# Optimization experiments

Measured on AMD Instinct MI355X. Metric: run time of the kernel, lower is better.

## Reference

```python
import jax, jax.numpy as jnp
import numpy as np

L, H, R, N, E = 6, 128, 64, 10000, 160000
SSILU_SCALE = 1.0 / 0.6  # ScaledSiLU
INV_SQRT_3 = 1.0 / np.sqrt(3.0)
INV_SQRT_H = 1.0 / np.sqrt(H)
INV_SQRT_2 = 1.0 / np.sqrt(2.0)


def ssilu(x):
    return jax.nn.silu(x) * SSILU_SCALE


def lnorm(x, w, b):
    m = x.mean(-1, keepdims=True)
    v = jnp.var(x, axis=-1, keepdims=True)
    return (x - m) * jax.lax.rsqrt(v + 1e-5) * w + b


def gated_block(x, v, wv1, wv2, wu1, bu1, wu2, bu2, hout):
    # GatedEquivariantBlock: x [N,Hin], v [N,3,Hin]
    vec1 = jnp.linalg.norm(jnp.einsum('nci,io->nco', v, wv1), axis=-2)  # [N,Hin]
    vec2 = jnp.einsum('nci,io->nco', v, wv2)                            # [N,3,hout]
    h = ssilu(jnp.concatenate([x, vec1], -1) @ wu1 + bu1) @ wu2 + bu2   # [N,2*hout]
    xs, xv = h[..., :hout], h[..., hout:]
    return ssilu(xs), xv[:, None, :] * vec2


def forward_impl(edge_index, x, vec, edge_rbf, edge_vector,
                 ln_w, ln_b, xp1_w, xp1_b, xp2_w, xp2_b, rbf_w, rbf_b,
                 vp_w, xv1_w, xv1_b, xv2_w, xv2_b,
                 we1, be1, we2, be2,
                 g1_v1, g1_v2, g1_u1, g1_u1b, g1_u2, g1_u2b,
                 g2_v1, g2_v2, g2_u1, g2_u1b, g2_u2, g2_u2b):
    src, dst = edge_index[0], edge_index[1]  # message flows src(j) -> dst(i)
    for l in range(L):
        # ---- PaiNNMessage ----
        xh = ssilu(lnorm(x, ln_w[l], ln_b[l]) @ xp1_w[l] + xp1_b[l]) @ xp2_w[l] + xp2_b[l]  # [N,3H]
        rbfh = edge_rbf @ rbf_w[l] + rbf_b[l]                                                # [E,3H]
        m = xh[src] * rbfh                                                                    # gather + elementwise
        mx = m[:, :H]
        m2 = m[:, H:2 * H] * INV_SQRT_3
        m3 = m[:, 2 * H:]
        mvec = (vec[src] * m2[:, None, :] + m3[:, None, :] * edge_vector[:, :, None]) * INV_SQRT_H  # [E,3,H]
        dx = jax.ops.segment_sum(mx, dst, num_segments=N)
        dvec = jax.ops.segment_sum(mvec, dst, num_segments=N)
        x = (x + dx) * INV_SQRT_2
        vec = vec + dvec
        # ---- PaiNNUpdate ----
        vp = jnp.einsum('nci,io->nco', vec, vp_w[l])  # [N,3,2H]
        v1, v2 = vp[..., :H], vp[..., H:]
        vec_dot = (v1 * v2).sum(axis=1) * INV_SQRT_H  # [N,H]
        vnorm = jnp.sqrt((v2 ** 2).sum(axis=-2) + 1e-8)
        h = ssilu(jnp.concatenate([x, vnorm], -1) @ xv1_w[l] + xv1_b[l]) @ xv2_w[l] + xv2_b[l]  # [N,3H]
        xu1, xu2, xu3 = h[:, :H], h[:, H:2 * H], h[:, 2 * H:]
        x = x + (xu1 + xu2 * vec_dot) * INV_SQRT_2
        vec = vec + xu3[:, None, :] * v1
        # ScaleFactor is identity without a scale file
    energy = ssilu(x @ we1 + be1) @ we2 + be2  # [N,1] per-atom energy
    fx, fv = gated_block(x, vec, g1_v1, g1_v2, g1_u1, g1_u1b, g1_u2, g1_u2b, H // 2)
    fx, fv = gated_block(fx, fv, g2_v1, g2_v2, g2_u1, g2_u1b, g2_u2, g2_u2b, 1)
    forces = fv[..., 0]  # [N,3]
    return jnp.concatenate([energy, forces], axis=-1)  # [N,4] packed (energy, fx, fy, fz)


def setup_inputs() -> dict:
    key = jax.random.key(0)
    ks = iter(jax.random.split(key, 64))
    nrm = lambda shape, s=0.05: jax.random.normal(next(ks), shape, jnp.float32) * s
    return dict(
        x=jax.random.normal(next(ks), (N, H), jnp.float32),
        vec=jax.random.normal(next(ks), (N, 3, H), jnp.float32),
        edge_index=jax.random.randint(next(ks), (2, E), 0, N),
        edge_rbf=jax.random.uniform(next(ks), (E, R), jnp.float32),
        edge_vector=jax.random.normal(next(ks), (E, 3), jnp.float32),
        ln_w=jnp.ones((L, H)), ln_b=jnp.zeros((L, H)),
        xp1_w=nrm((L, H, H)), xp1_b=jnp.zeros((L, H)),
        xp2_w=nrm((L, H, 3 * H)), xp2_b=jnp.zeros((L, 3 * H)),
        rbf_w=nrm((L, R, 3 * H)), rbf_b=jnp.zeros((L, 3 * H)),
        vp_w=nrm((L, H, 2 * H)),
        xv1_w=nrm((L, 2 * H, H)), xv1_b=jnp.zeros((L, H)),
        xv2_w=nrm((L, H, 3 * H)), xv2_b=jnp.zeros((L, 3 * H)),
        we1=nrm((H, H // 2)), be1=jnp.zeros((H // 2,)),
        we2=nrm((H // 2, 1)), be2=jnp.zeros((1,)),
        g1_v1=nrm((H, H)), g1_v2=nrm((H, H // 2)),
        g1_u1=nrm((2 * H, H)), g1_u1b=jnp.zeros((H,)),
        g1_u2=nrm((H, H)), g1_u2b=jnp.zeros((H,)),
        g2_v1=nrm((H // 2, H // 2)), g2_v2=nrm((H // 2, 1)),
        g2_u1=nrm((H, H // 2)), g2_u1b=jnp.zeros((H // 2,)),
        g2_u2=nrm((H // 2, 2)), g2_u2b=jnp.zeros((2,)),
    )


def reference(x, vec, edge_index, edge_rbf, edge_vector,
              ln_w, ln_b, xp1_w, xp1_b, xp2_w, xp2_b, rbf_w, rbf_b,
              vp_w, xv1_w, xv1_b, xv2_w, xv2_b,
              we1, be1, we2, be2,
              g1_v1, g1_v2, g1_u1, g1_u1b, g1_u2, g1_u2b,
              g2_v1, g2_v2, g2_u1, g2_u1b, g2_u2, g2_u2b):
    return forward_impl(edge_index, x, vec, edge_rbf, edge_vector,
                        ln_w, ln_b, xp1_w, xp1_b, xp2_w, xp2_b, rbf_w, rbf_b,
                        vp_w, xv1_w, xv1_b, xv2_w, xv2_b,
                        we1, be1, we2, be2,
                        g1_v1, g1_v2, g1_u1, g1_u1b, g1_u2, g1_u2b,
                        g2_v1, g2_v2, g2_u1, g2_u1b, g2_u2, g2_u2b)
```

## Files before the change

kernel.cpp:

```cpp
#include <hip/hip_runtime.h>
#include <hip/hip_bf16.h>

#define NN 10000
#define EE 160000
#define LL 6

#define INV_SQRT_3f  0.57735026919f
#define INV_SQRT_Hf  0.08838834764832f
#define INV_SQRT_2f  0.70710678118655f

typedef _Float16 half8 __attribute__((ext_vector_type(8)));
typedef float f32x4 __attribute__((ext_vector_type(4)));

#define WE1OFF   0
#define WV1OFF   8192
#define WV2OFF   24576
#define WU1OFF   32768
#define WU2OFF   65536
#define G2V1OFF  81920
#define G2U1OFF  86016
#define WFIN_SZ  94208

__device__ __forceinline__ float ssilu_f(float v){
  float s = 1.0f / (1.0f + __expf(-v));
  return v * s * 1.6666666666667f;
}
__device__ __forceinline__ float bcast(float v, int l){
  return __int_as_float(__builtin_amdgcn_readlane(__float_as_int(v), l));
}

__global__ __launch_bounds__(256) void k_hist(const int* __restrict__ edst, int* __restrict__ cnt){
  int i = blockIdx.x*256 + threadIdx.x;
  if (i < EE) atomicAdd(&cnt[edst[i]], 1);
}

__global__ __launch_bounds__(1024) void k_scan(const int* __restrict__ cnt,
                                               int* __restrict__ off, int* __restrict__ cur){
  __shared__ int ps[1024];
  int t = threadIdx.x;
  int base = t*10;
  int local[10];
  int s = 0;
  #pragma unroll
  for (int i=0;i<10;i++){
    int c = (base+i < NN) ? cnt[base+i] : 0;
    local[i] = s; s += c;
  }
  ps[t] = s;
  __syncthreads();
  for (int d=1; d<1024; d<<=1){
    int v = (t>=d) ? ps[t-d] : 0;
    __syncthreads();
    ps[t] += v;
    __syncthreads();
  }
  int pre = (t>0) ? ps[t-1] : 0;
  #pragma unroll
  for (int i=0;i<10;i++){
    int idx = base+i;
    if (idx < NN){ int o = pre + local[i]; off[idx]=o; cur[idx]=o; }
  }
  if (t==1023) off[NN] = ps[1023];
}

__global__ __launch_bounds__(256) void k_fill(const int* __restrict__ edst,
                                              int* __restrict__ cur, int* __restrict__ eord){
  int i = blockIdx.x*256 + threadIdx.x;
  if (i < EE){
    int d = edst[i];
    int p = atomicAdd(&cur[d], 1);
    eord[p] = i;
  }
}

__global__ __launch_bounds__(256) void k_sorta(const float* __restrict__ erbf,
                                               const int* __restrict__ eord, _Float16* __restrict__ eA){
  long i = (long)blockIdx.x*256 + threadIdx.x;
  if (i >= (long)EE*64) return;
  int j = i & 7, lane = (i >> 3) & 63, kh = (i >> 9) & 1;
  long tile = i >> 10;
  int e = eord[tile*16 + (lane&15)];
  eA[i] = (_Float16)erbf[(size_t)e*64 + kh*32 + (lane>>4)*8 + j];
}

__global__ __launch_bounds__(256) void k_sorte(const int* __restrict__ esrc, const float* __restrict__ evec,
                                               const int* __restrict__ eord, float4* __restrict__ es4){
  int p = blockIdx.x*256 + threadIdx.x;
  if (p >= EE) return;
  int e = eord[p];
  es4[p] = make_float4(evec[(size_t)e*3], evec[(size_t)e*3+1], evec[(size_t)e*3+2],
                       __int_as_float(esrc[e]));
}

__global__ __launch_bounds__(256) void k_packw(const float* __restrict__ w, _Float16* __restrict__ wf){
  int i = blockIdx.x*256 + threadIdx.x;
  if (i >= LL*24*2*64*8) return;
  int j    = i & 7;
  int lane = (i >> 3) & 63;
  int kh   = (i >> 9) & 1;
  int rest = i >> 10;
  int nb   = rest % 24;
  int l    = rest / 24;
  int k    = 32*kh + 8*(lane>>4) + j;
  int ch   = nb*16 + (lane&15);
  float v = w[((size_t)l*64 + k)*384 + ch];
  if (ch >= 128 && ch < 256) v *= INV_SQRT_3f;
  wf[i] = (_Float16)v;
}

__global__ __launch_bounds__(256) void k_packb(const float* __restrict__ b, float* __restrict__ bsc){
  int i = blockIdx.x*256 + threadIdx.x;
  if (i >= LL*384) return;
  int ch = i % 384;
  float v = b[i];
  if (ch >= 128 && ch < 256) v *= INV_SQRT_3f;
  bsc[i] = v;
}

struct PackTab {
  const float* s[40];
  _Float16* d[40];
  int K[40];
  int NO[40];
};
__global__ __launch_bounds__(256) void k_packall(PackTab tb){
  int e = blockIdx.y;
  int K = tb.K[e], NO = tb.NO[e];
  int tot = K*NO, KS = K >> 5;
  const float* s = tb.s[e];
  _Float16* d = tb.d[e];
  for (int i = blockIdx.x*256 + threadIdx.x; i < tot; i += gridDim.x*256){
    int j = i & 7, lane = (i >> 3) & 63, rest = i >> 9;
    int ks = rest % KS, nb = rest / KS;
    int k = ks*32 + (lane>>4)*8 + j, n = nb*16 + (lane&15);
    d[i] = (_Float16)s[(size_t)k*NO + n];
  }
}

__global__ __launch_bounds__(256) void k_cvt16(const float* __restrict__ v, _Float16* __restrict__ o, int n){
  int i = blockIdx.x*256 + threadIdx.x;
  if (i < n) o[i] = (_Float16)v[i];
}

__global__ __launch_bounds__(64) void k_gemm_rbfh(
    const _Float16* __restrict__ eA, const _Float16* __restrict__ wf,
    const float* __restrict__ bsc,
    _Float16* __restrict__ rbfh)
{
  int lane = threadIdx.x;
  int i0 = blockIdx.x * 64;
  int tg = blockIdx.x * 4;
  int ml = lane & 15, kg = lane >> 4;
  half8 a0[4], a1[4];
  #pragma unroll
  for (int tt = 0; tt < 4; tt++){
    a0[tt] = *(const half8*)(eA + ((size_t)((tg+tt)*2+0)*64 + lane)*8);
    a1[tt] = *(const half8*)(eA + ((size_t)((tg+tt)*2+1)*64 + lane)*8);
  }
  #pragma unroll 2
  for (int nb = 0; nb < 24; nb++){
    half8 b0 = *(const half8*)(wf + ((size_t)(nb*2+0)*64 + lane)*8);
    half8 b1 = *(const half8*)(wf + ((size_t)(nb*2+1)*64 + lane)*8);
    float bias = bsc[nb*16 + ml];
    #pragma unroll
    for (int tt = 0; tt < 4; tt++){
      f32x4 acc = {bias, bias, bias, bias};
      acc = __builtin_amdgcn_mfma_f32_16x16x32_f16(a0[tt], b0, acc, 0, 0, 0);
      acc = __builtin_amdgcn_mfma_f32_16x16x32_f16(a1[tt], b1, acc, 0, 0, 0);
      _Float16* orow = rbfh + (size_t)(i0 + tt*16)*384 + nb*16 + ml;
      #pragma unroll
      for (int r = 0; r < 4; r++)
        orow[(size_t)(kg*4 + r)*384] = (_Float16)acc[r];
    }
  }
}

__global__ __launch_bounds__(256) void k_xh_mfma(
    const float* __restrict__ x,
    const float* __restrict__ lnw, const float* __restrict__ lnb,
    const _Float16* __restrict__ wf1, const float* __restrict__ b1,
    const _Float16* __restrict__ wf2, const float* __restrict__ b2,
    _Float16* __restrict__ xh16)
{
  __shared__ _Float16 sA[32][136];
  __shared__ _Float16 sH[32][136];
  int t = threadIdx.x;
  int n0 = blockIdx.x * 32;
  {
    int nd = t >> 3, sb = t & 7;
    int node = n0 + nd;
    float v[16];
    float s = 0.f, ss = 0.f;
    if (node < NN){
      const float* xr = x + (size_t)node*128 + sb*16;
      #pragma unroll
      for (int g = 0; g < 4; g++){
        float4 q = *(const float4*)(xr + g*4);
        v[g*4+0]=q.x; v[g*4+1]=q.y; v[g*4+2]=q.z; v[g*4+3]=q.w;
      }
      #pragma unroll
      for (int u = 0; u < 16; u++){ s += v[u]; ss += v[u]*v[u]; }
    } else {
      #pragma unroll
      for (int u = 0; u < 16; u++) v[u] = 0.f;
    }
    #pragma unroll
    for (int o2 = 4; o2 > 0; o2 >>= 1){
      s  += __shfl_xor(s, o2, 8);
      ss += __shfl_xor(ss, o2, 8);
    }
    float mean = s * (1.0f/128.0f);
    float var  = ss * (1.0f/128.0f) - mean*mean;
    float rstd = rsqrtf(var + 1e-5f);
    #pragma unroll
    for (int u = 0; u < 16; u++){
      int h = sb*16 + u;
      sA[nd][h] = (node < NN) ? (_Float16)((v[u]-mean)*rstd*lnw[h] + lnb[h]) : (_Float16)0.f;
    }
  }
  __syncthreads();
  int lane = t & 63, w = t >> 6, ml = lane & 15, kg = lane >> 4;
  int mt = w >> 1;
  {
    half8 a[4];
    #pragma unroll
    for (int ks = 0; ks < 4; ks++)
      a[ks] = *(const half8*)&sA[mt*16 + ml][ks*32 + kg*8];
    float hout[4][4];
    #pragma unroll
    for (int nb4 = 0; nb4 < 4; nb4++){
      int nb = (w&1)*4 + nb4;
      float bias = b1[nb*16 + ml];
      f32x4 acc = {bias, bias, bias, bias};
      #pragma unroll
      for (int ks = 0; ks < 4; ks++)
        acc = __builtin_amdgcn_mfma_f32_16x16x32_f16(a[ks],
                *(const half8*)(wf1 + ((size_t)(nb*4+ks)*64 + lane)*8), acc, 0,0,0);
      #pragma unroll
      for (int r = 0; r < 4; r++) hout[nb4][r] = ssilu_f(acc[r]);
    }
    #pragma unroll
    for (int nb4 = 0; nb4 < 4; nb4++){
      int nb = (w&1)*4 + nb4;
      #pragma unroll
      for (int r = 0; r < 4; r++)
        sH[mt*16 + kg*4 + r][nb*16 + ml] = (_Float16)hout[nb4][r];
    }
  }
  __syncthreads();
  {
    half8 a[4];
    #pragma unroll
    for (int ks = 0; ks < 4; ks++)
      a[ks] = *(const half8*)&sH[mt*16 + ml][ks*32 + kg*8];
    #pragma unroll 4
    for (int nb12 = 0; nb12 < 12; nb12++){
      int nb = (w&1)*12 + nb12;
      float bias = b2[nb*16 + ml];
      f32x4 acc = {bias, bias, bias, bias};
      #pragma unroll
      for (int ks = 0; ks < 4; ks++)
        acc = __builtin_amdgcn_mfma_f32_16x16x32_f16(a[ks],
                *(const half8*)(wf2 + ((size_t)(nb*4+ks)*64 + lane)*8), acc, 0,0,0);
      #pragma unroll
      for (int r = 0; r < 4; r++){
        int m = mt*16 + kg*4 + r;
        int node = n0 + m;
        if (node < NN) xh16[(size_t)node*384 + nb*16 + ml] = (_Float16)acc[r];
      }
    }
  }
}

__global__ __launch_bounds__(256) void k_edge3(
    const _Float16* __restrict__ rbfh,
    const float4* __restrict__ es4, const int* __restrict__ off,
    const _Float16* __restrict__ xh16, const _Float16* __restrict__ vec16,
    float* __restrict__ dx, float* __restrict__ dvec)
{
  int t = threadIdx.x;
  int lane = t & 63;
  int n = blockIdx.x*4 + (t>>6);
  if (n >= NN) return;
  int o0 = off[n], o1 = off[n+1];
  float ax0 = 0.f, ax1 = 0.f;
  float av00=0.f, av01=0.f, av10=0.f, av11=0.f, av20=0.f, av21=0.f;
  #pragma unroll 2
  for (int p = o0; p < o1; p++){
    const _Float16* hr = rbfh + (size_t)p*384;
    float h0 = (float)hr[lane];
    float h1 = (float)hr[64+lane];
    float h2 = (float)hr[128+lane];
    float h3 = (float)hr[192+lane];
    float h4 = (float)hr[256+lane];
    float h5 = (float)hr[320+lane];
    float4 q = es4[p];
    int sN = __float_as_int(q.w);
    const _Float16* xr = xh16 + (size_t)sN*384;
    float m0  = h0 * (float)xr[lane];
    float m1  = h1 * (float)xr[64+lane];
    float m2a = h2 * (float)xr[128+lane];
    float m2b = h3 * (float)xr[192+lane];
    float m3a = h4 * (float)xr[256+lane];
    float m3b = h5 * (float)xr[320+lane];
    ax0 += m0; ax1 += m1;
    const _Float16* vr = vec16 + (size_t)sN*384;
    av00 = fmaf((float)vr[lane],     m2a, av00); av00 = fmaf(m3a, q.x, av00);
    av01 = fmaf((float)vr[64+lane],  m2b, av01); av01 = fmaf(m3b, q.x, av01);
    av10 = fmaf((float)vr[128+lane], m2a, av10); av10 = fmaf(m3a, q.y, av10);
    av11 = fmaf((float)vr[192+lane], m2b, av11); av11 = fmaf(m3b, q.y, av11);
    av20 = fmaf((float)vr[256+lane], m2a, av20); av20 = fmaf(m3a, q.z, av20);
    av21 = fmaf((float)vr[320+lane], m2b, av21); av21 = fmaf(m3b, q.z, av21);
  }
  float* dxr = dx + (size_t)n*128;
  dxr[lane] = ax0; dxr[64+lane] = ax1;
  float* dvr = dvec + (size_t)n*384;
  dvr[lane]     = av00 * INV_SQRT_Hf;
  dvr[64+lane]  = av01 * INV_SQRT_Hf;
  dvr[128+lane] = av10 * INV_SQRT_Hf;
  dvr[192+lane] = av11 * INV_SQRT_Hf;
  dvr[256+lane] = av20 * INV_SQRT_Hf;
  dvr[320+lane] = av21 * INV_SQRT_Hf;
}

__global__ __launch_bounds__(256) void k_node_mfma(
    float* __restrict__ xbuf, float* __restrict__ vbuf,
    const float* __restrict__ dx, const float* __restrict__ dvec,
    const _Float16* __restrict__ wfvp,
    const _Float16* __restrict__ wfxv1, const float* __restrict__ xv1_b,
    const _Float16* __restrict__ wfxv2, const float* __restrict__ xv2_b,
    _Float16* __restrict__ vec16)
{
  __shared__ _Float16 sV1[96][136];
  __shared__ _Float16 sCat[32][264];
  __shared__ _Float16 sVD[32][128];
  int t = threadIdx.x;
  int n0 = blockIdx.x * 32;
  int lane = t & 63, w = t >> 6, ml = lane & 15, kg = lane >> 4;
  int mt = w & 1, nbb = (w >> 1) * 4;
  float vd[4][4], vn[4][4];
  #pragma unroll
  for (int i=0;i<4;i++){
    #pragma unroll
    for (int r=0;r<4;r++){ vd[i][r]=0.f; vn[i][r]=0.f; }
  }
  int arow = n0 + mt*16 + ml;
  bool aok = arow < NN;
  for (int cd = 0; cd < 3; cd++){
    half8 a[4];
    #pragma unroll
    for (int ks = 0; ks < 4; ks++){
      if (aok){
        const float* vr = vbuf + (size_t)arow*384 + cd*128 + ks*32 + kg*8;
        const float* dr = dvec + (size_t)arow*384 + cd*128 + ks*32 + kg*8;
        float4 q0 = *(const float4*)(vr);
        float4 q1 = *(const float4*)(vr+4);
        float4 d0 = *(const float4*)(dr);
        float4 d1 = *(const float4*)(dr+4);
        a[ks][0]=(_Float16)(q0.x+d0.x); a[ks][1]=(_Float16)(q0.y+d0.y);
        a[ks][2]=(_Float16)(q0.z+d0.z); a[ks][3]=(_Float16)(q0.w+d0.w);
        a[ks][4]=(_Float16)(q1.x+d1.x); a[ks][5]=(_Float16)(q1.y+d1.y);
        a[ks][6]=(_Float16)(q1.z+d1.z); a[ks][7]=(_Float16)(q1.w+d1.w);
      } else {
        #pragma unroll
        for (int j=0;j<8;j++) a[ks][j] = (_Float16)0.f;
      }
    }
    #pragma unroll
    for (int nb4 = 0; nb4 < 4; nb4++){
      int nb1 = nbb + nb4;
      f32x4 acc1 = {0.f,0.f,0.f,0.f}, acc2 = {0.f,0.f,0.f,0.f};
      #pragma unroll
      for (int ks = 0; ks < 4; ks++){
        acc1 = __builtin_amdgcn_mfma_f32_16x16x32_f16(a[ks],
                 *(const half8*)(wfvp + ((size_t)(nb1*4+ks)*64 + lane)*8), acc1, 0,0,0);
        acc2 = __builtin_amdgcn_mfma_f32_16x16x32_f16(a[ks],
                 *(const half8*)(wfvp + ((size_t)((nb1+8)*4+ks)*64 + lane)*8), acc2, 0,0,0);
      }
      #pragma unroll
      for (int r = 0; r < 4; r++){
        float v1v = acc1[r], v2v = acc2[r];
        vd[nb4][r] += v1v*v2v;
        vn[nb4][r] += v2v*v2v;
        sV1[cd*32 + mt*16 + kg*4 + r][nb1*16 + ml] = (_Float16)v1v;
      }
    }
  }
  #pragma unroll
  for (int nb4 = 0; nb4 < 4; nb4++){
    #pragma unroll
    for (int r = 0; r < 4; r++){
      int m = mt*16 + kg*4 + r, c = (nbb+nb4)*16 + ml;
      sVD[m][c] = (_Float16)(vd[nb4][r] * INV_SQRT_Hf);
      sCat[m][128 + c] = (_Float16)sqrtf(vn[nb4][r] + 1e-8f);
    }
  }
  {
    int nd = t >> 3, sb = t & 7;
    int node = n0 + nd;
    if (node < NN){
      const float* xr = xbuf + (size_t)node*128 + sb*16;
      const float* dr = dx   + (size_t)node*128 + sb*16;
      #pragma unroll
      for (int g = 0; g < 4; g++){
        float4 qa = *(const float4*)(xr + g*4);
        float4 qb = *(const float4*)(dr + g*4);
        sCat[nd][sb*16+g*4+0] = (_Float16)((qa.x+qb.x)*INV_SQRT_2f);
        sCat[nd][sb*16+g*4+1] = (_Float16)((qa.y+qb.y)*INV_SQRT_2f);
        sCat[nd][sb*16+g*4+2] = (_Float16)((qa.z+qb.z)*INV_SQRT_2f);
        sCat[nd][sb*16+g*4+3] = (_Float16)((qa.w+qb.w)*INV_SQRT_2f);
      }
    } else {
      #pragma unroll
      for (int u = 0; u < 16; u++) sCat[nd][sb*16+u] = (_Float16)0.f;
    }
  }
  __syncthreads();
  float hreg[4][4];
  {
    half8 a[8];
    #pragma unroll
    for (int ks = 0; ks < 8; ks++)
      a[ks] = *(const half8*)&sCat[mt*16 + ml][ks*32 + kg*8];
    #pragma unroll
    for (int nb4 = 0; nb4 < 4; nb4++){
      int nb = (w>>1)*4 + nb4;
      float bias = xv1_b[nb*16 + ml];
      f32x4 acc = {bias, bias, bias, bias};
      #pragma unroll
      for (int ks = 0; ks < 8; ks++)
        acc = __builtin_amdgcn_mfma_f32_16x16x32_f16(a[ks],
                *(const half8*)(wfxv1 + ((size_t)(nb*8+ks)*64 + lane)*8), acc, 0,0,0);
      #pragma unroll
      for (int r = 0; r < 4; r++) hreg[nb4][r] = ssilu_f(acc[r]);
    }
  }
  __syncthreads();
  #pragma unroll
  for (int nb4 = 0; nb4 < 4; nb4++){
    int nb = (w>>1)*4 + nb4;
    #pragma unroll
    for (int r = 0; r < 4; r++)
      sCat[mt*16 + kg*4 + r][nb*16 + ml] = (_Float16)hreg[nb4][r];
  }
  __syncthreads();
  {
    half8 a[4];
    #pragma unroll
    for (int ks = 0; ks < 4; ks++)
      a[ks] = *(const half8*)&sCat[mt*16 + ml][ks*32 + kg*8];
    #pragma unroll 2
    for (int nb4 = 0; nb4 < 4; nb4++){
      int nbu = nbb + nb4;
      float b1v = xv2_b[nbu*16 + ml];
      float b2v = xv2_b[(nbu+8)*16 + ml];
      float b3v = xv2_b[(nbu+16)*16 + ml];
      f32x4 au1 = {b1v,b1v,b1v,b1v};
      f32x4 au2 = {b2v,b2v,b2v,b2v};
      f32x4 au3 = {b3v,b3v,b3v,b3v};
      #pragma unroll
      for (int ks = 0; ks < 4; ks++){
        au1 = __builtin_amdgcn_mfma_f32_16x16x32_f16(a[ks],
                *(const half8*)(wfxv2 + ((size_t)(nbu*4+ks)*64 + lane)*8), au1, 0,0,0);
        au2 = __builtin_amdgcn_mfma_f32_16x16x32_f16(a[ks],
                *(const half8*)(wfxv2 + ((size_t)((nbu+8)*4+ks)*64 + lane)*8), au2, 0,0,0);
        au3 = __builtin_amdgcn_mfma_f32_16x16x32_f16(a[ks],
                *(const half8*)(wfxv2 + ((size_t)((nbu+16)*4+ks)*64 + lane)*8), au3, 0,0,0);
      }
      #pragma unroll
      for (int r = 0; r < 4; r++){
        int m = mt*16 + kg*4 + r;
        int node = n0 + m;
        if (node >= NN) continue;
        int c = nbu*16 + ml;
        float xu1 = au1[r], xu2 = au2[r], xu3 = au3[r];
        float vdv = (float)sVD[m][c];
        size_t px = (size_t)node*128 + c;
        float xn = (xbuf[px] + dx[px]) * INV_SQRT_2f;
        xbuf[px] = xn + (xu1 + xu2*vdv) * INV_SQRT_2f;
        #pragma unroll
        for (int cd = 0; cd < 3; cd++){
          float v1v = (float)sV1[cd*32 + m][c];
          size_t pv = (size_t)node*384 + cd*128 + c;
          float vo = vbuf[pv] + dvec[pv] + xu3*v1v;
          vbuf[pv] = vo;
          vec16[pv] = (_Float16)vo;
        }
      }
    }
  }
}

__global__ __launch_bounds__(256) void k_final(
    const float* __restrict__ x, const float* __restrict__ vec,
    const _Float16* __restrict__ wfin,
    const float* __restrict__ be1, const float* __restrict__ we2, const float* __restrict__ be2,
    const float* __restrict__ u1b, const float* __restrict__ u2b,
    const float* __restrict__ g2v2, const float* __restrict__ g2u1b, const float* __restrict__ g2u2,
    const float* __restrict__ g2u2b,
    float* __restrict__ out)
{
  __shared__ _Float16 sCat[32][264];
  __shared__ _Float16 sV2[3][32][72];
  __shared__ _Float16 sH[32][136];
  __shared__ _Float16 sFV[3][32][72];
  __shared__ _Float16 sE1[32][72];
  __shared__ float sR[3][32];
  int t = threadIdx.x;
  int n0 = blockIdx.x * 32;
  int lane = t & 63, w = t >> 6, ml = lane & 15, kg = lane >> 4;
  int mt = w & 1, nh = w >> 1;

  {
    int nd = t >> 3, sb = t & 7;
    int node = n0 + nd;
    if (node < NN){
      const float* xr = x + (size_t)node*128 + sb*16;
      #pragma unroll
      for (int g = 0; g < 4; g++){
        float4 q = *(const float4*)(xr + g*4);
        sCat[nd][sb*16+g*4+0]=(_Float16)q.x; sCat[nd][sb*16+g*4+1]=(_Float16)q.y;
        sCat[nd][sb*16+g*4+2]=(_Float16)q.z; sCat[nd][sb*16+g*4+3]=(_Float16)q.w;
      }
    } else {
      #pragma unroll
      for (int u = 0; u < 16; u++) sCat[nd][sb*16+u] = (_Float16)0.f;
    }
  }
  {
    int arow = n0 + mt*16 + ml;
    bool aok = arow < NN;
    float n1sq[4][4];
    #pragma unroll
    for (int i=0;i<4;i++){
      #pragma unroll
      for (int r=0;r<4;r++) n1sq[i][r]=0.f;
    }
    for (int cd = 0; cd < 3; cd++){
      half8 a[4];
      #pragma unroll
      for (int ks = 0; ks < 4; ks++){
        if (aok){
          const float* vr = vec + (size_t)arow*384 + cd*128 + ks*32 + kg*8;
          float4 q0 = *(const float4*)(vr);
          float4 q1 = *(const float4*)(vr+4);
          a[ks][0]=(_Float16)q0.x; a[ks][1]=(_Float16)q0.y; a[ks][2]=(_Float16)q0.z; a[ks][3]=(_Float16)q0.w;
          a[ks][4]=(_Float16)q1.x; a[ks][5]=(_Float16)q1.y; a[ks][6]=(_Float16)q1.z; a[ks][7]=(_Float16)q1.w;
        } else {
          #pragma unroll
          for (int j=0;j<8;j++) a[ks][j] = (_Float16)0.f;
        }
      }
      #pragma unroll
      for (int nb4 = 0; nb4 < 4; nb4++){
        int nb = nh*4 + nb4;
        f32x4 acc = {0.f,0.f,0.f,0.f};
        #pragma unroll
        for (int ks = 0; ks < 4; ks++)
          acc = __builtin_amdgcn_mfma_f32_16x16x32_f16(a[ks],
                  *(const half8*)(wfin + WV1OFF + ((size_t)(nb*4+ks)*64 + lane)*8), acc, 0,0,0);
        #pragma unroll
        for (int r = 0; r < 4; r++) n1sq[nb4][r] += acc[r]*acc[r];
      }
      #pragma unroll
      for (int q = 0; q < 2; q++){
        int nb = nh*2 + q;
        f32x4 acc = {0.f,0.f,0.f,0.f};
        #pragma unroll
        for (int ks = 0; ks < 4; ks++)
          acc = __builtin_amdgcn_mfma_f32_16x16x32_f16(a[ks],
                  *(const half8*)(wfin + WV2OFF + ((size_t)(nb*4+ks)*64 + lane)*8), acc, 0,0,0);
        #pragma unroll
        for (int r = 0; r < 4; r++)
          sV2[cd][mt*16 + kg*4 + r][nb*16 + ml] = (_Float16)acc[r];
      }
    }
    #pragma unroll
    for (int nb4 = 0; nb4 < 4; nb4++){
      #pragma unroll
      for (int r = 0; r < 4; r++)
        sCat[mt*16 + kg*4 + r][128 + nh*64 + nb4*16 + ml] = (_Float16)sqrtf(n1sq[nb4][r]);
    }
  }
  __syncthreads();
  {
    half8 a[8];
    #pragma unroll
    for (int ks = 0; ks < 8; ks++)
      a[ks] = *(const half8*)&sCat[mt*16 + ml][ks*32 + kg*8];
    #pragma unroll
    for (int q = 0; q < 2; q++){
      int nb = nh*2 + q;
      float bias = be1[nb*16 + ml];
      f32x4 acc = {bias, bias, bias, bias};
      #pragma unroll
      for (int ks = 0; ks < 4; ks++)
        acc = __builtin_amdgcn_mfma_f32_16x16x32_f16(a[ks],
                *(const half8*)(wfin + WE1OFF + ((size_t)(nb*4+ks)*64 + lane)*8), acc, 0,0,0);
      #pragma unroll
      for (int r = 0; r < 4; r++)
        sE1[mt*16 + kg*4 + r][nb*16 + ml] = (_Float16)ssilu_f(acc[r]);
    }
    #pragma unroll
    for (int nb4 = 0; nb4 < 4; nb4++){
      int nb = nh*4 + nb4;
      float bias = u1b[nb*16 + ml];
      f32x4 acc = {bias, bias, bias, bias};
      #pragma unroll
      for (int ks = 0; ks < 8; ks++)
        acc = __builtin_amdgcn_mfma_f32_16x16x32_f16(a[ks],
                *(const half8*)(wfin + WU1OFF + ((size_t)(nb*8+ks)*64 + lane)*8), acc, 0,0,0);
      #pragma unroll
      for (int r = 0; r < 4; r++)
        sH[mt*16 + kg*4 + r][nb*16 + ml] = (_Float16)ssilu_f(acc[r]);
    }
  }
  __syncthreads();
  {
    half8 a[4];
    #pragma unroll
    for (int ks = 0; ks < 4; ks++)
      a[ks] = *(const half8*)&sH[mt*16 + ml][ks*32 + kg*8];
    #pragma unroll
    for (int nb4 = 0; nb4 < 4; nb4++){
      int nb = nh*4 + nb4;
      float bias = u2b[nb*16 + ml];
      f32x4 acc = {bias, bias, bias, bias};
      #pragma unroll
      for (int ks = 0; ks < 4; ks++)
        acc = __builtin_amdgcn_mfma_f32_16x16x32_f16(a[ks],
                *(const half8*)(wfin + WU2OFF + ((size_t)(nb*4+ks)*64 + lane)*8), acc, 0,0,0);
      int c = nb*16 + ml;
      #pragma unroll
      for (int r = 0; r < 4; r++){
        int m = mt*16 + kg*4 + r;
        if (c < 64){
          sCat[m][c] = (_Float16)ssilu_f(acc[r]);
        } else {
          float xv = acc[r];
          #pragma unroll
          for (int cd = 0; cd < 3; cd++)
            sFV[cd][m][c-64] = (_Float16)(xv * (float)sV2[cd][m][c-64]);
        }
      }
    }
    float wev = we2[lane];
    #pragma unroll
    for (int i = 0; i < 8; i++){
      int nd = w*8 + i;
      float v = (float)sE1[nd][lane] * wev;
      #pragma unroll
      for (int o2 = 32; o2 > 0; o2 >>= 1) v += __shfl_xor(v, o2, 64);
      int node = n0 + nd;
      if (lane == 0 && node < NN) out[(size_t)node*4 + 0] = v + be2[0];
    }
  }
  __syncthreads();
  {
    float n1sq[2][4];
    #pragma unroll
    for (int q=0;q<2;q++){
      #pragma unroll
      for (int r=0;r<4;r++) n1sq[q][r]=0.f;
    }
    for (int cd = 0; cd < 3; cd++){
      half8 a[2];
      #pragma unroll
      for (int ks = 0; ks < 2; ks++)
        a[ks] = *(const half8*)&sFV[cd][mt*16 + ml][ks*32 + kg*8];
      #pragma unroll
      for (int q = 0; q < 2; q++){
        int nb = nh*2 + q;
        f32x4 acc = {0.f,0.f,0.f,0.f};
        #pragma unroll
        for (int ks = 0; ks < 2; ks++)
          acc = __builtin_amdgcn_mfma_f32_16x16x32_f16(a[ks],
                  *(const half8*)(wfin + G2V1OFF + ((size_t)(nb*2+ks)*64 + lane)*8), acc, 0,0,0);
        #pragma unroll
        for (int r = 0; r < 4; r++) n1sq[q][r] += acc[r]*acc[r];
      }
    }
    #pragma unroll
    for (int q = 0; q < 2; q++){
      #pragma unroll
      for (int r = 0; r < 4; r++)
        sCat[mt*16 + kg*4 + r][64 + (nh*2+q)*16 + ml] = (_Float16)sqrtf(n1sq[q][r]);
    }
    float g2v = g2v2[lane];
    #pragma unroll
    for (int i = 0; i < 8; i++){
      int nd = w*8 + i;
      #pragma unroll
      for (int cd = 0; cd < 3; cd++){
        float v = (float)sFV[cd][nd][lane] * g2v;
        #pragma unroll
        for (int o2 = 32; o2 > 0; o2 >>= 1) v += __shfl_xor(v, o2, 64);
        if (lane == 0) sR[cd][nd] = v;
      }
    }
  }
  __syncthreads();
  {
    half8 a[4];
    #pragma unroll
    for (int ks = 0; ks < 4; ks++)
      a[ks] = *(const half8*)&sCat[mt*16 + ml][ks*32 + kg*8];
    #pragma unroll
    for (int q = 0; q < 2; q++){
      int nb = nh*2 + q;
      float bias = g2u1b[nb*16 + ml];
      f32x4 acc = {bias, bias, bias, bias};
      #pragma unroll
      for (int ks = 0; ks < 4; ks++)
        acc = __builtin_amdgcn_mfma_f32_16x16x32_f16(a[ks],
                *(const half8*)(wfin + G2U1OFF + ((size_t)(nb*4+ks)*64 + lane)*8), acc, 0,0,0);
      #pragma unroll
      for (int r = 0; r < 4; r++)
        sE1[mt*16 + kg*4 + r][nb*16 + ml] = (_Float16)ssilu_f(acc[r]);
    }
  }
  __syncthreads();
  {
    float g2w = g2u2[lane*2 + 1];
    #pragma unroll
    for (int i = 0; i < 8; i++){
      int nd = w*8 + i;
      float v = (float)sE1[nd][lane] * g2w;
      #pragma unroll
      for (int o2 = 32; o2 > 0; o2 >>= 1) v += __shfl_xor(v, o2, 64);
      int node = n0 + nd;
      if (lane == 0 && node < NN){
        float h21 = v + g2u2b[1];
        out[(size_t)node*4 + 1] = h21 * sR[0][nd];
        out[(size_t)node*4 + 2] = h21 * sR[1][nd];
        out[(size_t)node*4 + 3] = h21 * sR[2][nd];
      }
    }
  }
}

extern "C" void kernel_launch(void* const* d_in, const int* in_sizes, int n_in,
                              void* d_out, int out_size, void* d_ws, size_t ws_size,
                              hipStream_t stream)
{
  const float* x_in   = (const float*)d_in[0];
  const float* vec_in = (const float*)d_in[1];
  const int*   eidx   = (const int*)d_in[2];
  const float* erbf   = (const float*)d_in[3];
  const float* evec   = (const float*)d_in[4];
  const float* ln_w  = (const float*)d_in[5];
  const float* ln_b  = (const float*)d_in[6];
  const float* xp1_w = (const float*)d_in[7];
  const float* xp1_b = (const float*)d_in[8];
  const float* xp2_w = (const float*)d_in[9];
  const float* xp2_b = (const float*)d_in[10];
  const float* rbf_w = (const float*)d_in[11];
  const float* rbf_b = (const float*)d_in[12];
  const float* vp_w  = (const float*)d_in[13];
  const float* xv1_w = (const float*)d_in[14];
  const float* xv1_b = (const float*)d_in[15];
  const float* xv2_w = (const float*)d_in[16];
  const float* xv2_b = (const float*)d_in[17];
  const float* we1 = (const float*)d_in[18];
  const float* be1 = (const float*)d_in[19];
  const float* we2 = (const float*)d_in[20];
  const float* be2 = (const float*)d_in[21];
  const float* g1_v1 = (const float*)d_in[22];
  const float* g1_v2 = (const float*)d_in[23];
  const float* g1_u1 = (const float*)d_in[24];
  const float* g1_u1b = (const float*)d_in[25];
  const float* g1_u2 = (const float*)d_in[26];
  const float* g1_u2b = (const float*)d_in[27];
  const float* g2_v1 = (const float*)d_in[28];
  const float* g2_v2 = (const float*)d_in[29];
  const float* g2_u1 = (const float*)d_in[30];
  const float* g2_u1b = (const float*)d_in[31];
  const float* g2_u2 = (const float*)d_in[32];
  const float* g2_u2b = (const float*)d_in[33];
  float* out = (float*)d_out;

  char* base = (char*)d_ws;
  size_t o = 0;
  auto alloc = [&](size_t bytes) -> char* {
    char* p = base + o;
    o = (o + bytes + 255) & ~(size_t)255;
    return p;
  };
  float* x_cur   = (float*)alloc((size_t)NN*128*4);
  float* vec_cur = (float*)alloc((size_t)NN*384*4);
  float* dx      = (float*)alloc((size_t)NN*128*4);
  float* dvec    = (float*)alloc((size_t)NN*384*4);
  _Float16* xh16 = (_Float16*)alloc((size_t)NN*384*2);
  _Float16* vec16= (_Float16*)alloc((size_t)NN*384*2);
  int*   eord    = (int*)alloc((size_t)EE*4);
  int*   off     = (int*)alloc((size_t)(NN+1)*4);
  _Float16* wf   = (_Float16*)alloc((size_t)LL*24576*2);
  float* bsc     = (float*)alloc((size_t)LL*384*4);
  _Float16* wfn  = (_Float16*)alloc((size_t)LL*180224*2);
  _Float16* wfin = (_Float16*)alloc((size_t)WFIN_SZ*2);
  _Float16* eA   = (_Float16*)alloc((size_t)EE*64*2);
  float4* es4    = (float4*)alloc((size_t)EE*16);
  _Float16* rbfh = (_Float16*)alloc((size_t)EE*384*2);
  int* cnt = (int*)dx;
  int* cur = cnt + NN;

  hipMemcpyAsync(x_cur, x_in, sizeof(float)*(size_t)NN*128, hipMemcpyDeviceToDevice, stream);
  hipMemcpyAsync(vec_cur, vec_in, sizeof(float)*(size_t)NN*384, hipMemcpyDeviceToDevice, stream);

  const int* esrc = eidx;
  const int* edst = eidx + EE;

  hipMemsetAsync(cnt, 0, sizeof(int)*NN, stream);
  k_hist<<<(EE+255)/256, 256, 0, stream>>>(edst, cnt);
  k_scan<<<1, 1024, 0, stream>>>(cnt, off, cur);
  k_fill<<<(EE+255)/256, 256, 0, stream>>>(edst, cur, eord);
  k_sorta<<<(EE*64+255)/256, 256, 0, stream>>>(erbf, eord, eA);
  k_sorte<<<(EE+255)/256, 256, 0, stream>>>(esrc, evec, eord, es4);
  k_packw<<<(LL*24576+255)/256, 256, 0, stream>>>(rbf_w, wf);
  k_packb<<<(LL*384+255)/256, 256, 0, stream>>>(rbf_b, bsc);
  k_cvt16<<<(NN*384+255)/256, 256, 0, stream>>>(vec_in, vec16, NN*384);

  {
    PackTab tb;
    for (int l = 0; l < LL; l++){
      _Float16* wb = wfn + (size_t)l*180224;
      tb.s[l*5+0] = xp1_w + (size_t)l*128*128; tb.d[l*5+0] = wb;          tb.K[l*5+0]=128; tb.NO[l*5+0]=128;
      tb.s[l*5+1] = xp2_w + (size_t)l*128*384; tb.d[l*5+1] = wb+16384;    tb.K[l*5+1]=128; tb.NO[l*5+1]=384;
      tb.s[l*5+2] = vp_w  + (size_t)l*128*256; tb.d[l*5+2] = wb+65536;    tb.K[l*5+2]=128; tb.NO[l*5+2]=256;
      tb.s[l*5+3] = xv1_w + (size_t)l*256*128; tb.d[l*5+3] = wb+98304;    tb.K[l*5+3]=256; tb.NO[l*5+3]=128;
      tb.s[l*5+4] = xv2_w + (size_t)l*128*384; tb.d[l*5+4] = wb+131072;   tb.K[l*5+4]=128; tb.NO[l*5+4]=384;
    }
    tb.s[30] = we1;   tb.d[30] = wfin + WE1OFF;  tb.K[30]=128; tb.NO[30]=64;
    tb.s[31] = g1_v1; tb.d[31] = wfin + WV1OFF;  tb.K[31]=128; tb.NO[31]=128;
    tb.s[32] = g1_v2; tb.d[32] = wfin + WV2OFF;  tb.K[32]=128; tb.NO[32]=64;
    tb.s[33] = g1_u1; tb.d[33] = wfin + WU1OFF;  tb.K[33]=256; tb.NO[33]=128;
    tb.s[34] = g1_u2; tb.d[34] = wfin + WU2OFF;  tb.K[34]=128; tb.NO[34]=128;
    tb.s[35] = g2_v1; tb.d[35] = wfin + G2V1OFF; tb.K[35]=64;  tb.NO[35]=64;
    tb.s[36] = g2_u1; tb.d[36] = wfin + G2U1OFF; tb.K[36]=128; tb.NO[36]=64;
    k_packall<<<dim3(24, 37), 256, 0, stream>>>(tb);
  }

  for (int l = 0; l < LL; l++){
    _Float16* wb = wfn + (size_t)l*180224;
    k_xh_mfma<<<(NN+31)/32, 256, 0, stream>>>(x_cur, ln_w + l*128, ln_b + l*128,
        wb, xp1_b + l*128, wb+16384, xp2_b + l*384, xh16);
    k_gemm_rbfh<<<EE/64, 64, 0, stream>>>(eA, wf + (size_t)l*24576,
        bsc + (size_t)l*384, rbfh);
    k_edge3<<<NN/4, 256, 0, stream>>>(rbfh, es4, off, xh16, vec16, dx, dvec);
    k_node_mfma<<<(NN+31)/32, 256, 0, stream>>>(x_cur, vec_cur, dx, dvec,
        wb+65536, wb+98304, xv1_b + l*128, wb+131072, xv2_b + l*384, vec16);
  }
  k_final<<<(NN+31)/32, 256, 0, stream>>>(x_cur, vec_cur, wfin,
      be1, we2, be2, g1_u1b, g1_u2b, g2_v2, g2_u1b, g2_u2, g2_u2b, out);
}
```

Measured before the change: 972.6 us.

## Merge xh and rbfh GEMMs into one launch; store dx/dvec in fp16

The node-feature GEMM (xh) and the per-edge RBF GEMM now run in one launch. The first 313 blocks handle the node tiles and the remaining blocks each run four 64-thread rbfh tile groups. This removes a launch per layer and lets the two independent GEMMs overlap. The dx and dvec aggregation buffers also drop from fp32 to fp16, halving their write and read traffic between the edge and node kernels at some cost in accumulated precision.

```diff
diff --git a/kernel.cpp b/kernel.cpp
--- a/kernel.cpp
+++ b/kernel.cpp
@@ -24,9 +24,6 @@
 __device__ __forceinline__ float ssilu_f(float v){
   float s = 1.0f / (1.0f + __expf(-v));
   return v * s * 1.6666666666667f;
-}
-__device__ __forceinline__ float bcast(float v, int l){
-  return __int_as_float(__builtin_amdgcn_readlane(__float_as_int(v), l));
 }
 
 __global__ __launch_bounds__(256) void k_hist(const int* __restrict__ edst, int* __restrict__ cnt){
@@ -142,49 +139,48 @@
   if (i < n) o[i] = (_Float16)v[i];
 }
 
-__global__ __launch_bounds__(64) void k_gemm_rbfh(
-    const _Float16* __restrict__ eA, const _Float16* __restrict__ wf,
-    const float* __restrict__ bsc,
-    _Float16* __restrict__ rbfh)
-{
-  int lane = threadIdx.x;
-  int i0 = blockIdx.x * 64;
-  int tg = blockIdx.x * 4;
-  int ml = lane & 15, kg = lane >> 4;
-  half8 a0[4], a1[4];
-  #pragma unroll
-  for (int tt = 0; tt < 4; tt++){
-    a0[tt] = *(const half8*)(eA + ((size_t)((tg+tt)*2+0)*64 + lane)*8);
-    a1[tt] = *(const half8*)(eA + ((size_t)((tg+tt)*2+1)*64 + lane)*8);
-  }
-  #pragma unroll 2
-  for (int nb = 0; nb < 24; nb++){
-    half8 b0 = *(const half8*)(wf + ((size_t)(nb*2+0)*64 + lane)*8);
-    half8 b1 = *(const half8*)(wf + ((size_t)(nb*2+1)*64 + lane)*8);
-    float bias = bsc[nb*16 + ml];
-    #pragma unroll
-    for (int tt = 0; tt < 4; tt++){
-      f32x4 acc = {bias, bias, bias, bias};
-      acc = __builtin_amdgcn_mfma_f32_16x16x32_f16(a0[tt], b0, acc, 0, 0, 0);
-      acc = __builtin_amdgcn_mfma_f32_16x16x32_f16(a1[tt], b1, acc, 0, 0, 0);
-      _Float16* orow = rbfh + (size_t)(i0 + tt*16)*384 + nb*16 + ml;
-      #pragma unroll
-      for (int r = 0; r < 4; r++)
-        orow[(size_t)(kg*4 + r)*384] = (_Float16)acc[r];
-    }
-  }
-}
-
-__global__ __launch_bounds__(256) void k_xh_mfma(
+__global__ __launch_bounds__(256) void k_xhgemm(
     const float* __restrict__ x,
     const float* __restrict__ lnw, const float* __restrict__ lnb,
     const _Float16* __restrict__ wf1, const float* __restrict__ b1,
     const _Float16* __restrict__ wf2, const float* __restrict__ b2,
-    _Float16* __restrict__ xh16)
+    _Float16* __restrict__ xh16,
+    const _Float16* __restrict__ eA, const _Float16* __restrict__ wf,
+    const float* __restrict__ bsc, _Float16* __restrict__ rbfh)
 {
   __shared__ _Float16 sA[32][136];
   __shared__ _Float16 sH[32][136];
   int t = threadIdx.x;
+  if (blockIdx.x >= 313){
+    int ob = (blockIdx.x - 313)*4 + (t >> 6);
+    int lane = t & 63;
+    int i0 = ob * 64;
+    int tg = ob * 4;
+    int ml = lane & 15, kg = lane >> 4;
+    half8 a0[4], a1[4];
+    #pragma unroll
+    for (int tt = 0; tt < 4; tt++){
+      a0[tt] = *(const half8*)(eA + ((size_t)((tg+tt)*2+0)*64 + lane)*8);
+      a1[tt] = *(const half8*)(eA + ((size_t)((tg+tt)*2+1)*64 + lane)*8);
+    }
+    #pragma unroll 2
+    for (int nb = 0; nb < 24; nb++){
+      half8 b0 = *(const half8*)(wf + ((size_t)(nb*2+0)*64 + lane)*8);
+      half8 b1h = *(const half8*)(wf + ((size_t)(nb*2+1)*64 + lane)*8);
+      float bias = bsc[nb*16 + ml];
+      #pragma unroll
+      for (int tt = 0; tt < 4; tt++){
+        f32x4 acc = {bias, bias, bias, bias};
+        acc = __builtin_amdgcn_mfma_f32_16x16x32_f16(a0[tt], b0, acc, 0, 0, 0);
+        acc = __builtin_amdgcn_mfma_f32_16x16x32_f16(a1[tt], b1h, acc, 0, 0, 0);
+        _Float16* orow = rbfh + (size_t)(i0 + tt*16)*384 + nb*16 + ml;
+        #pragma unroll
+        for (int r = 0; r < 4; r++)
+          orow[(size_t)(kg*4 + r)*384] = (_Float16)acc[r];
+      }
+    }
+    return;
+  }
   int n0 = blockIdx.x * 32;
   {
     int nd = t >> 3, sb = t & 7;
@@ -276,7 +272,7 @@
     const _Float16* __restrict__ rbfh,
     const float4* __restrict__ es4, const int* __restrict__ off,
     const _Float16* __restrict__ xh16, const _Float16* __restrict__ vec16,
-    float* __restrict__ dx, float* __restrict__ dvec)
+    _Float16* __restrict__ dx, _Float16* __restrict__ dvec)
 {
   int t = threadIdx.x;
   int lane = t & 63;
@@ -312,20 +308,20 @@
     av20 = fmaf((float)vr[256+lane], m2a, av20); av20 = fmaf(m3a, q.z, av20);
     av21 = fmaf((float)vr[320+lane], m2b, av21); av21 = fmaf(m3b, q.z, av21);
   }
-  float* dxr = dx + (size_t)n*128;
-  dxr[lane] = ax0; dxr[64+lane] = ax1;
-  float* dvr = dvec + (size_t)n*384;
-  dvr[lane]     = av00 * INV_SQRT_Hf;
-  dvr[64+lane]  = av01 * INV_SQRT_Hf;
-  dvr[128+lane] = av10 * INV_SQRT_Hf;
-  dvr[192+lane] = av11 * INV_SQRT_Hf;
-  dvr[256+lane] = av20 * INV_SQRT_Hf;
-  dvr[320+lane] = av21 * INV_SQRT_Hf;
+  _Float16* dxr = dx + (size_t)n*128;
+  dxr[lane] = (_Float16)ax0; dxr[64+lane] = (_Float16)ax1;
+  _Float16* dvr = dvec + (size_t)n*384;
+  dvr[lane]     = (_Float16)(av00 * INV_SQRT_Hf);
+  dvr[64+lane]  = (_Float16)(av01 * INV_SQRT_Hf);
+  dvr[128+lane] = (_Float16)(av10 * INV_SQRT_Hf);
+  dvr[192+lane] = (_Float16)(av11 * INV_SQRT_Hf);
+  dvr[256+lane] = (_Float16)(av20 * INV_SQRT_Hf);
+  dvr[320+lane] = (_Float16)(av21 * INV_SQRT_Hf);
 }
 
 __global__ __launch_bounds__(256) void k_node_mfma(
     float* __restrict__ xbuf, float* __restrict__ vbuf,
-    const float* __restrict__ dx, const float* __restrict__ dvec,
+    const _Float16* __restrict__ dx, const _Float16* __restrict__ dvec,
     const _Float16* __restrict__ wfvp,
     const _Float16* __restrict__ wfxv1, const float* __restrict__ xv1_b,
     const _Float16* __restrict__ wfxv2, const float* __restrict__ xv2_b,
@@ -352,15 +348,14 @@
     for (int ks = 0; ks < 4; ks++){
       if (aok){
         const float* vr = vbuf + (size_t)arow*384 + cd*128 + ks*32 + kg*8;
-        const float* dr = dvec + (size_t)arow*384 + cd*128 + ks*32 + kg*8;
+        const _Float16* dr = dvec + (size_t)arow*384 + cd*128 + ks*32 + kg*8;
         float4 q0 = *(const float4*)(vr);
         float4 q1 = *(const float4*)(vr+4);
-        float4 d0 = *(const float4*)(dr);
-        float4 d1 = *(const float4*)(dr+4);
-        a[ks][0]=(_Float16)(q0.x+d0.x); a[ks][1]=(_Float16)(q0.y+d0.y);
-        a[ks][2]=(_Float16)(q0.z+d0.z); a[ks][3]=(_Float16)(q0.w+d0.w);
-        a[ks][4]=(_Float16)(q1.x+d1.x); a[ks][5]=(_Float16)(q1.y+d1.y);
-        a[ks][6]=(_Float16)(q1.z+d1.z); a[ks][7]=(_Float16)(q1.w+d1.w);
+        half8 dh = *(const half8*)(dr);
+        a[ks][0]=(_Float16)(q0.x+(float)dh[0]); a[ks][1]=(_Float16)(q0.y+(float)dh[1]);
+        a[ks][2]=(_Float16)(q0.z+(float)dh[2]); a[ks][3]=(_Float16)(q0.w+(float)dh[3]);
+        a[ks][4]=(_Float16)(q1.x+(float)dh[4]); a[ks][5]=(_Float16)(q1.y+(float)dh[5]);
+        a[ks][6]=(_Float16)(q1.z+(float)dh[6]); a[ks][7]=(_Float16)(q1.w+(float)dh[7]);
       } else {
         #pragma unroll
         for (int j=0;j<8;j++) a[ks][j] = (_Float16)0.f;
@@ -400,15 +395,20 @@
     int node = n0 + nd;
     if (node < NN){
       const float* xr = xbuf + (size_t)node*128 + sb*16;
-      const float* dr = dx   + (size_t)node*128 + sb*16;
+      const _Float16* dr = dx + (size_t)node*128 + sb*16;
+      half8 da = *(const half8*)(dr);
+      half8 db = *(const half8*)(dr+8);
       #pragma unroll
       for (int g = 0; g < 4; g++){
         float4 qa = *(const float4*)(xr + g*4);
-        float4 qb = *(const float4*)(dr + g*4);
-        sCat[nd][sb*16+g*4+0] = (_Float16)((qa.x+qb.x)*INV_SQRT_2f);
-        sCat[nd][sb*16+g*4+1] = (_Float16)((qa.y+qb.y)*INV_SQRT_2f);
-        sCat[nd][sb*16+g*4+2] = (_Float16)((qa.z+qb.z)*INV_SQRT_2f);
-        sCat[nd][sb*16+g*4+3] = (_Float16)((qa.w+qb.w)*INV_SQRT_2f);
+        float d0 = (float)((g<2)?da[g*4+0]:db[(g-2)*4+0]);
+        float d1 = (float)((g<2)?da[g*4+1]:db[(g-2)*4+1]);
+        float d2 = (float)((g<2)?da[g*4+2]:db[(g-2)*4+2]);
+        float d3 = (float)((g<2)?da[g*4+3]:db[(g-2)*4+3]);
+        sCat[nd][sb*16+g*4+0] = (_Float16)((qa.x+d0)*INV_SQRT_2f);
+        sCat[nd][sb*16+g*4+1] = (_Float16)((qa.y+d1)*INV_SQRT_2f);
+        sCat[nd][sb*16+g*4+2] = (_Float16)((qa.z+d2)*INV_SQRT_2f);
+        sCat[nd][sb*16+g*4+3] = (_Float16)((qa.w+d3)*INV_SQRT_2f);
       }
     } else {
       #pragma unroll
@@ -476,13 +476,13 @@
         float xu1 = au1[r], xu2 = au2[r], xu3 = au3[r];
         float vdv = (float)sVD[m][c];
         size_t px = (size_t)node*128 + c;
-        float xn = (xbuf[px] + dx[px]) * INV_SQRT_2f;
+        float xn = (xbuf[px] + (float)dx[px]) * INV_SQRT_2f;
         xbuf[px] = xn + (xu1 + xu2*vdv) * INV_SQRT_2f;
         #pragma unroll
         for (int cd = 0; cd < 3; cd++){
           float v1v = (float)sV1[cd*32 + m][c];
           size_t pv = (size_t)node*384 + cd*128 + c;
-          float vo = vbuf[pv] + dvec[pv] + xu3*v1v;
+          float vo = vbuf[pv] + (float)dvec[pv] + xu3*v1v;
           vbuf[pv] = vo;
           vec16[pv] = (_Float16)vo;
         }
@@ -788,8 +788,8 @@
   };
   float* x_cur   = (float*)alloc((size_t)NN*128*4);
   float* vec_cur = (float*)alloc((size_t)NN*384*4);
-  float* dx      = (float*)alloc((size_t)NN*128*4);
-  float* dvec    = (float*)alloc((size_t)NN*384*4);
+  _Float16* dx   = (_Float16*)alloc((size_t)NN*128*2);
+  _Float16* dvec = (_Float16*)alloc((size_t)NN*384*2);
   _Float16* xh16 = (_Float16*)alloc((size_t)NN*384*2);
   _Float16* vec16= (_Float16*)alloc((size_t)NN*384*2);
   int*   eord    = (int*)alloc((size_t)EE*4);
@@ -842,10 +842,9 @@
 
   for (int l = 0; l < LL; l++){
     _Float16* wb = wfn + (size_t)l*180224;
-    k_xh_mfma<<<(NN+31)/32, 256, 0, stream>>>(x_cur, ln_w + l*128, ln_b + l*128,
-        wb, xp1_b + l*128, wb+16384, xp2_b + l*384, xh16);
-    k_gemm_rbfh<<<EE/64, 64, 0, stream>>>(eA, wf + (size_t)l*24576,
-        bsc + (size_t)l*384, rbfh);
+    k_xhgemm<<<938, 256, 0, stream>>>(x_cur, ln_w + l*128, ln_b + l*128,
+        wb, xp1_b + l*128, wb+16384, xp2_b + l*384, xh16,
+        eA, wf + (size_t)l*24576, bsc + (size_t)l*384, rbfh);
     k_edge3<<<NN/4, 256, 0, stream>>>(rbfh, es4, off, xh16, vec16, dx, dvec);
     k_node_mfma<<<(NN+31)/32, 256, 0, stream>>>(x_cur, vec_cur, dx, dvec,
         wb+65536, wb+98304, xv1_b + l*128, wb+131072, xv2_b + l*384, vec16);
```

Result: faster. 888.7 us, median of 2 (-8.6%).
